# Optimization experiments

Measured on AMD Instinct MI355X. Metric: run time of the kernel, lower is better.

## Reference

```python
import jax, jax.numpy as jnp
import numpy as np

N_NODES = 50000
N_EDGES = 500000
N_GRAPHS = 256
D_IN, D_H1, D_H2, D_H3, D_OUT = 768, 256, 128, 64, 2


def _glorot(key, shape):
    fan_in, fan_out = shape[1], shape[0]
    lim = float(np.sqrt(6.0 / (fan_in + fan_out)))
    return jax.random.uniform(key, shape, jnp.float32, -lim, lim)


def setup_inputs() -> dict:
    key = jax.random.key(0)
    ks = jax.random.split(key, 12)
    x = jax.random.normal(ks[0], (N_NODES, D_IN), jnp.float32)
    edge_index = jax.random.randint(ks[1], (2, N_EDGES), 0, N_NODES, jnp.int64)
    batch = jnp.sort(jax.random.randint(ks[2], (N_NODES,), 0, N_GRAPHS, jnp.int64))
    return {
        "x": x,
        "edge_index": edge_index,
        "batch": batch,
        # SAGEConv1: out = lin_l(mean_aggr) + lin_r(x); bias only on lin_l (PyG default)
        "W1_l": _glorot(ks[3], (D_H1, D_IN)),
        "b1_l": jnp.zeros((D_H1,), jnp.float32),
        "W1_r": _glorot(ks[4], (D_H1, D_IN)),
        # SAGEConv2
        "W2_l": _glorot(ks[5], (D_H2, D_H1)),
        "b2_l": jnp.zeros((D_H2,), jnp.float32),
        "W2_r": _glorot(ks[6], (D_H2, D_H1)),
        # MLP head
        "W3": _glorot(ks[7], (D_H3, D_H2)),
        "b3": jnp.zeros((D_H3,), jnp.float32),
        "W4": _glorot(ks[8], (D_OUT, D_H3)),
        "b4": jnp.zeros((D_OUT,), jnp.float32),
    }


def _sage_conv(x, src, dst, deg_inv, W_l, b_l, W_r):
    # mean aggregation of neighbor features: scatter-add then divide by in-degree
    aggr = jax.ops.segment_sum(x[src], dst, num_segments=N_NODES)  # [N, d]
    aggr = aggr * deg_inv[:, None]
    return aggr @ W_l.T + b_l + x @ W_r.T


def reference(x, edge_index, batch, W1_l, b1_l, W1_r, W2_l, b2_l, W2_r, W3, b3, W4, b4):
    src, dst = edge_index[0], edge_index[1]
    deg = jax.ops.segment_sum(jnp.ones((N_EDGES,), x.dtype), dst, num_segments=N_NODES)
    deg_inv = jnp.where(deg > 0, 1.0 / jnp.maximum(deg, 1.0), 0.0)

    h = jax.nn.relu(_sage_conv(x, src, dst, deg_inv, W1_l, b1_l, W1_r))
    h = jax.nn.relu(_sage_conv(h, src, dst, deg_inv, W2_l, b2_l, W2_r))

    # global_mean_pool over graph ids
    pooled = jax.ops.segment_sum(h, batch, num_segments=N_GRAPHS)  # [G, 128]
    cnt = jax.ops.segment_sum(jnp.ones((N_NODES,), h.dtype), batch, num_segments=N_GRAPHS)
    pooled = pooled / jnp.maximum(cnt, 1.0)[:, None]

    # dropout is identity in eval mode
    h = pooled @ W3.T + b3
    h = h @ W4.T + b4
    return jax.nn.softmax(h, axis=-1)
```

## Files before the change

kernel.cpp:

```cpp
#include <hip/hip_runtime.h>
#include <cstdint>
#include <cstddef>

#define N_NODES 50000
#define N_EDGES 500000
#define N_GRAPHS 256
#define D_IN 768
#define D_H1 256
#define D_H2 128

typedef __attribute__((ext_vector_type(8))) __bf16 bf16x8;
typedef __attribute__((ext_vector_type(4))) float f32x4;

__device__ __forceinline__ float bf2f(uint32_t u) {
    union { uint32_t i; float f; } v; v.i = u << 16; return v.f;
}
__device__ __forceinline__ uint32_t f2bf(float f) {
    union { float f; uint32_t i; } v; v.f = f;
    uint32_t u = v.i;
    return (u + 0x7FFFu + ((u >> 16) & 1u)) >> 16;
}

__global__ void k_packA(const float* __restrict__ in, uint16_t* __restrict__ out,
                        int nchunks, int KT, int K) {
    int c = blockIdx.x * 256 + threadIdx.x;
    if (c >= nchunks) return;
    int l = c & 63, t = c >> 6;
    int kt = t % KT, mt = t / KT;
    int fr = l & 15, fq = l >> 4;
    const float* p = in + (size_t)(mt * 16 + fr) * K + kt * 32 + fq * 8;
    float4 u = *(const float4*)p, v = *(const float4*)(p + 4);
    uint4 o;
    o.x = f2bf(u.x) | (f2bf(u.y) << 16);
    o.y = f2bf(u.z) | (f2bf(u.w) << 16);
    o.z = f2bf(v.x) | (f2bf(v.y) << 16);
    o.w = f2bf(v.z) | (f2bf(v.w) << 16);
    *(uint4*)(out + (size_t)c * 8) = o;
}

__global__ void k_packW(const float* __restrict__ inL, const float* __restrict__ inR,
                        uint16_t* __restrict__ out, int rowsL, int nchunks, int KT, int K) {
    int c = blockIdx.x * 256 + threadIdx.x;
    if (c >= nchunks) return;
    int l = c & 63, t = c >> 6;
    int kt = t % KT, mt = t / KT;
    int fr = l & 15, fq = l >> 4;
    int row = mt * 16 + fr;
    const float* src = (row < rowsL) ? (inL + (size_t)row * K) : (inR + (size_t)(row - rowsL) * K);
    const float* p = src + kt * 32 + fq * 8;
    float4 u = *(const float4*)p, v = *(const float4*)(p + 4);
    uint4 o;
    o.x = f2bf(u.x) | (f2bf(u.y) << 16);
    o.y = f2bf(u.z) | (f2bf(u.w) << 16);
    o.z = f2bf(v.x) | (f2bf(v.y) << 16);
    o.w = f2bf(v.z) | (f2bf(v.w) << 16);
    *(uint4*)(out + (size_t)c * 8) = o;
}

__global__ void k_hist(const int* __restrict__ dst, int* __restrict__ deg, int n) {
    int e = blockIdx.x * blockDim.x + threadIdx.x;
    if (e < n) atomicAdd(&deg[dst[e]], 1);
}

__global__ void k_scan1(const int* __restrict__ deg, int* __restrict__ row_ex,
                        int* __restrict__ bsum, int n) {
    __shared__ int buf[256];
    int t = threadIdx.x, i = blockIdx.x * 256 + t;
    int v = (i < n) ? deg[i] : 0;
    buf[t] = v; __syncthreads();
    for (int off = 1; off < 256; off <<= 1) {
        int u = (t >= off) ? buf[t - off] : 0;
        __syncthreads(); buf[t] += u; __syncthreads();
    }
    if (i < n) row_ex[i] = buf[t] - v;
    if (t == 255) bsum[blockIdx.x] = buf[255];
}
__global__ void k_scan2(const int* __restrict__ bsum, int* __restrict__ boff, int nb) {
    __shared__ int buf[256];
    int t = threadIdx.x;
    int v = (t < nb) ? bsum[t] : 0;
    buf[t] = v; __syncthreads();
    for (int off = 1; off < 256; off <<= 1) {
        int u = (t >= off) ? buf[t - off] : 0;
        __syncthreads(); buf[t] += u; __syncthreads();
    }
    if (t < nb) boff[t] = buf[t] - v;
}
__global__ void k_scan3(const int* __restrict__ deg, const int* __restrict__ boff,
                        int* __restrict__ row_start, float* __restrict__ deg_inv, int n) {
    int i = blockIdx.x * 256 + threadIdx.x;
    if (i < n) {
        row_start[i] += boff[blockIdx.x];
        int d = deg[i];
        deg_inv[i] = (d > 0) ? (1.0f / (float)d) : 0.0f;
    }
    if (blockIdx.x == 0 && threadIdx.x == 0) row_start[n] = N_EDGES;
}

__global__ void k_fill(const int* __restrict__ src, const int* __restrict__ dst,
                       const int* __restrict__ row_start, int* __restrict__ cursor,
                       int* __restrict__ csr_src, int n) {
    int e = blockIdx.x * blockDim.x + threadIdx.x;
    if (e < n) {
        int d = dst[e];
        int pos = row_start[d] + atomicAdd(&cursor[d], 1);
        csr_src[pos] = src[e];
    }
}

__global__ __launch_bounds__(256, 2) void k_mgemm(
    const uint16_t* __restrict__ Ap, const uint16_t* __restrict__ Bp,
    uint16_t* __restrict__ C, int M, int N, int KT)
{
    const int tid = threadIdx.x;
    const int wave = tid >> 6, lane = tid & 63;
    const int fr = lane & 15, fq = lane >> 4;
    const int bn = blockIdx.x * 256, bm = blockIdx.y * 128;
    const int wm = (wave >> 1) * 64, wn = (wave & 1) * 128;
    const int mtiles = (M + 15) >> 4;

    const bf16x8* ap[4];
    const bf16x8* bp[8];
    #pragma unroll
    for (int mi = 0; mi < 4; ++mi) {
        int mt = ((bm + wm) >> 4) + mi;
        if (mt > mtiles - 1) mt = mtiles - 1;
        ap[mi] = (const bf16x8*)Ap + (size_t)mt * KT * 64 + lane;
    }
    #pragma unroll
    for (int ni = 0; ni < 8; ++ni) {
        int nt = ((bn + wn) >> 4) + ni;
        bp[ni] = (const bf16x8*)Bp + (size_t)nt * KT * 64 + lane;
    }

    f32x4 acc[4][8] = {};
    bf16x8 a0[4], b0[8], a1[4], b1[8];

    auto lA = [&](int kt, bf16x8* d) {
        #pragma unroll
        for (int mi = 0; mi < 4; ++mi) d[mi] = ap[mi][kt * 64];
    };
    auto lB = [&](int kt, bf16x8* d) {
        #pragma unroll
        for (int ni = 0; ni < 8; ++ni) d[ni] = bp[ni][kt * 64];
    };
    auto step = [&](bf16x8* a, bf16x8* b) {
        #pragma unroll
        for (int mi = 0; mi < 4; ++mi)
            #pragma unroll
            for (int ni = 0; ni < 8; ++ni)
                acc[mi][ni] = __builtin_amdgcn_mfma_f32_16x16x32_bf16(
                    a[mi], b[ni], acc[mi][ni], 0, 0, 0);
    };

    lA(0, a0); lB(0, b0);
    for (int ks = 0; ks < KT; ks += 2) {
        lA(ks + 1, a1); lB(ks + 1, b1);
        step(a0, b0);
        if (ks + 2 < KT) { lA(ks + 2, a0); lB(ks + 2, b0); }
        step(a1, b1);
    }

    #pragma unroll
    for (int mi = 0; mi < 4; ++mi) {
        #pragma unroll
        for (int r = 0; r < 4; ++r) {
            int row = bm + wm + mi * 16 + fq * 4 + r;
            if (row >= M) continue;
            #pragma unroll
            for (int ni = 0; ni < 8; ++ni) {
                int col = bn + wn + ni * 16 + fr;
                C[(size_t)row * N + col] = (uint16_t)f2bf(acc[mi][ni][r]);
            }
        }
    }
}

__global__ __launch_bounds__(256) void k_agg1(
    const uint16_t* __restrict__ y, const int* __restrict__ row_start,
    const int* __restrict__ csr, const float* __restrict__ deg_inv,
    const float* __restrict__ bias, uint16_t* __restrict__ h1p)
{
    int node = blockIdx.x * 8 + (threadIdx.x >> 5);
    if (node >= N_NODES) return;
    int c = threadIdx.x & 31;
    int s = row_start[node], e = row_start[node + 1];
    float a[8] = {};
    int p = s;
    for (; p + 1 < e; p += 2) {
        uint4 t0 = *(const uint4*)(y + (size_t)csr[p] * 512 + c * 8);
        uint4 t1 = *(const uint4*)(y + (size_t)csr[p + 1] * 512 + c * 8);
        a[0] += bf2f(t0.x & 0xFFFF) + bf2f(t1.x & 0xFFFF);
        a[1] += bf2f(t0.x >> 16)    + bf2f(t1.x >> 16);
        a[2] += bf2f(t0.y & 0xFFFF) + bf2f(t1.y & 0xFFFF);
        a[3] += bf2f(t0.y >> 16)    + bf2f(t1.y >> 16);
        a[4] += bf2f(t0.z & 0xFFFF) + bf2f(t1.z & 0xFFFF);
        a[5] += bf2f(t0.z >> 16)    + bf2f(t1.z >> 16);
        a[6] += bf2f(t0.w & 0xFFFF) + bf2f(t1.w & 0xFFFF);
        a[7] += bf2f(t0.w >> 16)    + bf2f(t1.w >> 16);
    }
    if (p < e) {
        uint4 t0 = *(const uint4*)(y + (size_t)csr[p] * 512 + c * 8);
        a[0] += bf2f(t0.x & 0xFFFF); a[1] += bf2f(t0.x >> 16);
        a[2] += bf2f(t0.y & 0xFFFF); a[3] += bf2f(t0.y >> 16);
        a[4] += bf2f(t0.z & 0xFFFF); a[5] += bf2f(t0.z >> 16);
        a[6] += bf2f(t0.w & 0xFFFF); a[7] += bf2f(t0.w >> 16);
    }
    float w = deg_inv[node];
    uint4 tx = *(const uint4*)(y + (size_t)node * 512 + 256 + c * 8);
    float4 b0 = *(const float4*)(bias + c * 8);
    float4 b1 = *(const float4*)(bias + c * 8 + 4);
    float v0 = fmaxf(a[0] * w + bf2f(tx.x & 0xFFFF) + b0.x, 0.f);
    float v1 = fmaxf(a[1] * w + bf2f(tx.x >> 16)    + b0.y, 0.f);
    float v2 = fmaxf(a[2] * w + bf2f(tx.y & 0xFFFF) + b0.z, 0.f);
    float v3 = fmaxf(a[3] * w + bf2f(tx.y >> 16)    + b0.w, 0.f);
    float v4 = fmaxf(a[4] * w + bf2f(tx.z & 0xFFFF) + b1.x, 0.f);
    float v5 = fmaxf(a[5] * w + bf2f(tx.z >> 16)    + b1.y, 0.f);
    float v6 = fmaxf(a[6] * w + bf2f(tx.w & 0xFFFF) + b1.z, 0.f);
    float v7 = fmaxf(a[7] * w + bf2f(tx.w >> 16)    + b1.w, 0.f);
    uint4 o;
    o.x = f2bf(v0) | (f2bf(v1) << 16);
    o.y = f2bf(v2) | (f2bf(v3) << 16);
    o.z = f2bf(v4) | (f2bf(v5) << 16);
    o.w = f2bf(v6) | (f2bf(v7) << 16);
    uint32_t addr = (((node >> 4) * 8 + (c >> 2)) * 64 + (c & 3) * 16 + (node & 15));
    *(uint4*)(h1p + (size_t)addr * 8) = o;
}

__global__ __launch_bounds__(256) void k_agg2(
    const uint16_t* __restrict__ y, const int* __restrict__ row_start,
    const int* __restrict__ csr, const float* __restrict__ deg_inv,
    const float* __restrict__ bias, float* __restrict__ out)
{
    int node = blockIdx.x * 4 + (threadIdx.x >> 6);
    if (node >= N_NODES) return;
    int lane = threadIdx.x & 63;
    int s = row_start[node], e = row_start[node + 1];
    float a0 = 0.f, a1 = 0.f;
    int p = s;
    for (; p + 1 < e; p += 2) {
        uint32_t t0 = *(const uint32_t*)(y + (size_t)csr[p] * 256 + lane * 2);
        uint32_t t1 = *(const uint32_t*)(y + (size_t)csr[p + 1] * 256 + lane * 2);
        a0 += bf2f(t0 & 0xFFFF) + bf2f(t1 & 0xFFFF);
        a1 += bf2f(t0 >> 16)    + bf2f(t1 >> 16);
    }
    if (p < e) {
        uint32_t t0 = *(const uint32_t*)(y + (size_t)csr[p] * 256 + lane * 2);
        a0 += bf2f(t0 & 0xFFFF);
        a1 += bf2f(t0 >> 16);
    }
    float w = deg_inv[node];
    uint32_t tx = *(const uint32_t*)(y + (size_t)node * 256 + 128 + lane * 2);
    float2 b = *(const float2*)(bias + lane * 2);
    float2 o;
    o.x = fmaxf(a0 * w + bf2f(tx & 0xFFFF) + b.x, 0.f);
    o.y = fmaxf(a1 * w + bf2f(tx >> 16)    + b.y, 0.f);
    *(float2*)(out + (size_t)node * 128 + lane * 2) = o;
}

__global__ void k_pool(const float* __restrict__ h2, const int* __restrict__ batch,
                       float* __restrict__ pooled)
{
    int g = blockIdx.x;
    __shared__ int s_lo, s_hi;
    if (threadIdx.x == 0) {
        int lo = 0, hi = N_NODES;
        while (lo < hi) { int m = (lo + hi) >> 1; if (batch[m] < g) lo = m + 1; else hi = m; }
        s_lo = lo;
        int lo2 = lo, hi2 = N_NODES;
        while (lo2 < hi2) { int m = (lo2 + hi2) >> 1; if (batch[m] < g + 1) lo2 = m + 1; else hi2 = m; }
        s_hi = lo2;
    }
    __syncthreads();
    int dim = threadIdx.x;
    float sum = 0.f;
    for (int i = s_lo; i < s_hi; ++i) sum += h2[(size_t)i * D_H2 + dim];
    int cnt = s_hi - s_lo;
    pooled[g * D_H2 + dim] = sum / (float)(cnt > 0 ? cnt : 1);
}

__global__ void k_head(const float* __restrict__ pooled, const float* __restrict__ W3,
                       const float* __restrict__ b3, const float* __restrict__ W4,
                       const float* __restrict__ b4, float* __restrict__ out)
{
    int g = blockIdx.x;
    int j = threadIdx.x;
    __shared__ float p[128];
    __shared__ float hid[64];
    __shared__ float logit[2];
    p[j] = pooled[g * 128 + j];
    p[j + 64] = pooled[g * 128 + 64 + j];
    __syncthreads();
    float s = b3[j];
    #pragma unroll 4
    for (int k = 0; k < 128; ++k) s = fmaf(p[k], W3[j * 128 + k], s);
    hid[j] = s;
    __syncthreads();
    if (j < 2) {
        float l = b4[j];
        for (int k = 0; k < 64; ++k) l = fmaf(hid[k], W4[j * 64 + k], l);
        logit[j] = l;
    }
    __syncthreads();
    if (j == 0) {
        float m = fmaxf(logit[0], logit[1]);
        float e0 = expf(logit[0] - m), e1 = expf(logit[1] - m);
        float inv = 1.0f / (e0 + e1);
        out[g * 2 + 0] = e0 * inv;
        out[g * 2 + 1] = e1 * inv;
    }
}

extern "C" void kernel_launch(void* const* d_in, const int* in_sizes, int n_in,
                              void* d_out, int out_size, void* d_ws, size_t ws_size,
                              hipStream_t stream)
{
    const float* x     = (const float*)d_in[0];
    const int*   ei    = (const int*)d_in[1];
    const int*   batch = (const int*)d_in[2];
    const float* W1l   = (const float*)d_in[3];
    const float* b1l   = (const float*)d_in[4];
    const float* W1r   = (const float*)d_in[5];
    const float* W2l   = (const float*)d_in[6];
    const float* b2l   = (const float*)d_in[7];
    const float* W2r   = (const float*)d_in[8];
    const float* W3    = (const float*)d_in[9];
    const float* b3    = (const float*)d_in[10];
    const float* W4    = (const float*)d_in[11];
    const float* b4    = (const float*)d_in[12];
    float* out = (float*)d_out;

    const int* e_src = ei;
    const int* e_dst = ei + N_EDGES;

    char* ws = (char*)d_ws;
    size_t off = 0;
    auto alloc = [&](size_t bytes) -> void* {
        void* p = ws + off;
        off = (off + bytes + 255) & ~(size_t)255;
        return p;
    };
    int*      deg       = (int*)alloc((size_t)N_NODES * 4);
    int*      row_start = (int*)alloc((size_t)(N_NODES + 1) * 4);
    int*      cursor    = (int*)alloc((size_t)N_NODES * 4);
    int*      csr_src   = (int*)alloc((size_t)N_EDGES * 4);
    float*    deg_inv   = (float*)alloc((size_t)N_NODES * 4);
    int*      bsum      = (int*)alloc(256 * 4);
    int*      boff      = (int*)alloc(256 * 4);
    float*    pooled    = (float*)alloc((size_t)N_GRAPHS * D_H2 * 4);
    uint16_t* W1p       = (uint16_t*)alloc((size_t)512 * 768 * 2);
    uint16_t* W2p       = (uint16_t*)alloc((size_t)256 * 256 * 2);
    uint16_t* xp        = (uint16_t*)alloc((size_t)N_NODES * D_IN * 2);
    uint16_t* y1        = (uint16_t*)alloc((size_t)N_NODES * 512 * 2);
    uint16_t* h1p       = (uint16_t*)alloc((size_t)N_NODES * 256 * 2);

    uint16_t* y2 = xp;
    float*    h2 = (float*)(xp + (size_t)N_NODES * 256);

    hipMemsetAsync(deg, 0, (size_t)N_NODES * 4, stream);
    hipMemsetAsync(cursor, 0, (size_t)N_NODES * 4, stream);

    k_hist<<<(N_EDGES + 255) / 256, 256, 0, stream>>>(e_dst, deg, N_EDGES);
    int nscan = (N_NODES + 255) / 256;
    k_scan1<<<nscan, 256, 0, stream>>>(deg, row_start, bsum, N_NODES);
    k_scan2<<<1, 256, 0, stream>>>(bsum, boff, nscan);
    k_scan3<<<nscan, 256, 0, stream>>>(deg, boff, row_start, deg_inv, N_NODES);
    k_fill<<<(N_EDGES + 255) / 256, 256, 0, stream>>>(e_src, e_dst, row_start, cursor, csr_src, N_EDGES);

    int ncA = 3125 * 24 * 64;
    k_packA<<<(ncA + 255) / 256, 256, 0, stream>>>(x, xp, ncA, 24, 768);
    int ncW1 = 32 * 24 * 64;
    k_packW<<<(ncW1 + 255) / 256, 256, 0, stream>>>(W1l, W1r, W1p, 256, ncW1, 24, 768);
    int ncW2 = 16 * 8 * 64;
    k_packW<<<(ncW2 + 255) / 256, 256, 0, stream>>>(W2l, W2r, W2p, 128, ncW2, 8, 256);

    dim3 g1(2, (N_NODES + 127) / 128);
    k_mgemm<<<g1, 256, 0, stream>>>(xp, W1p, y1, N_NODES, 512, 24);
    k_agg1<<<(N_NODES + 7) / 8, 256, 0, stream>>>(y1, row_start, csr_src, deg_inv, b1l, h1p);

    dim3 g2(1, (N_NODES + 127) / 128);
    k_mgemm<<<g2, 256, 0, stream>>>(h1p, W2p, y2, N_NODES, 256, 8);
    k_agg2<<<(N_NODES + 3) / 4, 256, 0, stream>>>(y2, row_start, csr_src, deg_inv, b2l, h2);

    k_pool<<<N_GRAPHS, 128, 0, stream>>>(h2, batch, pooled);
    k_head<<<N_GRAPHS, 64, 0, stream>>>(pooled, W3, b3, W4, b4, out);
}
```

Before: 529.1 us.

## Fuse preprocessing kernels and overlap CSR fill with first GEMM

Several small kernels are merged into fewer launches. The pack kernels and the degree histogram share one grid, scan2 and scan3 become one kernel, and pool and head become one kernel. The CSR fill now runs as extra blocks inside the first GEMM launch so the two overlap, and the GEMM output is split into separate left and right halves with a grouped block order for reuse. The goal is to cut launch overhead and idle tails between small kernels; the cost is added branch complexity and heterogeneous blocks sharing one launch.

New measurement: 486.8 us. -8.0%, faster.

```diff
diff --git a/kernel.cpp b/kernel.cpp
--- a/kernel.cpp
+++ b/kernel.cpp
@@ -21,14 +21,8 @@
     return (u + 0x7FFFu + ((u >> 16) & 1u)) >> 16;
 }
 
-__global__ void k_packA(const float* __restrict__ in, uint16_t* __restrict__ out,
-                        int nchunks, int KT, int K) {
-    int c = blockIdx.x * 256 + threadIdx.x;
-    if (c >= nchunks) return;
-    int l = c & 63, t = c >> 6;
-    int kt = t % KT, mt = t / KT;
-    int fr = l & 15, fq = l >> 4;
-    const float* p = in + (size_t)(mt * 16 + fr) * K + kt * 32 + fq * 8;
+__device__ __forceinline__ void pack_chunk(const float* __restrict__ p,
+                                           uint16_t* __restrict__ out, int c) {
     float4 u = *(const float4*)p, v = *(const float4*)(p + 4);
     uint4 o;
     o.x = f2bf(u.x) | (f2bf(u.y) << 16);
@@ -38,28 +32,45 @@
     *(uint4*)(out + (size_t)c * 8) = o;
 }
 
-__global__ void k_packW(const float* __restrict__ inL, const float* __restrict__ inR,
-                        uint16_t* __restrict__ out, int rowsL, int nchunks, int KT, int K) {
-    int c = blockIdx.x * 256 + threadIdx.x;
-    if (c >= nchunks) return;
-    int l = c & 63, t = c >> 6;
-    int kt = t % KT, mt = t / KT;
-    int fr = l & 15, fq = l >> 4;
-    int row = mt * 16 + fr;
-    const float* src = (row < rowsL) ? (inL + (size_t)row * K) : (inR + (size_t)(row - rowsL) * K);
-    const float* p = src + kt * 32 + fq * 8;
-    float4 u = *(const float4*)p, v = *(const float4*)(p + 4);
-    uint4 o;
-    o.x = f2bf(u.x) | (f2bf(u.y) << 16);
-    o.y = f2bf(u.z) | (f2bf(u.w) << 16);
-    o.z = f2bf(v.x) | (f2bf(v.y) << 16);
-    o.w = f2bf(v.z) | (f2bf(v.w) << 16);
-    *(uint4*)(out + (size_t)c * 8) = o;
-}
-
-__global__ void k_hist(const int* __restrict__ dst, int* __restrict__ deg, int n) {
-    int e = blockIdx.x * blockDim.x + threadIdx.x;
-    if (e < n) atomicAdd(&deg[dst[e]], 1);
+#define PACKA_BLKS 18750
+#define PACKW1_BLKS 192
+#define PACKW2_BLKS 32
+#define HIST_BLKS 1954
+__global__ __launch_bounds__(256) void k_pack_hist(
+    const float* __restrict__ x, uint16_t* __restrict__ xp,
+    const float* __restrict__ W1l, const float* __restrict__ W1r, uint16_t* __restrict__ W1p,
+    const float* __restrict__ W2l, const float* __restrict__ W2r, uint16_t* __restrict__ W2p,
+    const int* __restrict__ e_dst, int* __restrict__ deg)
+{
+    int b = blockIdx.x;
+    if (b < PACKA_BLKS) {
+        int c = b * 256 + threadIdx.x;
+        int l = c & 63, t = c >> 6;
+        int kt = t % 24, mt = t / 24;
+        int fr = l & 15, fq = l >> 4;
+        pack_chunk(x + (size_t)(mt * 16 + fr) * 768 + kt * 32 + fq * 8, xp, c);
+    } else if (b < PACKA_BLKS + PACKW1_BLKS) {
+        int c = (b - PACKA_BLKS) * 256 + threadIdx.x;
+        int l = c & 63, t = c >> 6;
+        int kt = t % 24, mt = t / 24;
+        int fr = l & 15, fq = l >> 4;
+        int row = mt * 16 + fr;
+        const float* src = (row < 256) ? (W1l + (size_t)row * 768)
+                                       : (W1r + (size_t)(row - 256) * 768);
+        pack_chunk(src + kt * 32 + fq * 8, W1p, c);
+    } else if (b < PACKA_BLKS + PACKW1_BLKS + PACKW2_BLKS) {
+        int c = (b - PACKA_BLKS - PACKW1_BLKS) * 256 + threadIdx.x;
+        int l = c & 63, t = c >> 6;
+        int kt = t % 8, mt = t / 8;
+        int fr = l & 15, fq = l >> 4;
+        int row = mt * 16 + fr;
+        const float* src = (row < 128) ? (W2l + (size_t)row * 256)
+                                       : (W2r + (size_t)(row - 128) * 256);
+        pack_chunk(src + kt * 32 + fq * 8, W2p, c);
+    } else {
+        int e = (b - PACKA_BLKS - PACKW1_BLKS - PACKW2_BLKS) * 256 + threadIdx.x;
+        if (e < N_EDGES) atomicAdd(&deg[e_dst[e]], 1);
+    }
 }
 
 __global__ void k_scan1(const int* __restrict__ deg, int* __restrict__ row_ex,
@@ -75,7 +86,9 @@
     if (i < n) row_ex[i] = buf[t] - v;
     if (t == 255) bsum[blockIdx.x] = buf[255];
 }
-__global__ void k_scan2(const int* __restrict__ bsum, int* __restrict__ boff, int nb) {
+__global__ void k_scan23(const int* __restrict__ deg, const int* __restrict__ bsum,
+                         int* __restrict__ row_start, float* __restrict__ deg_inv,
+                         int n, int nb) {
     __shared__ int buf[256];
     int t = threadIdx.x;
     int v = (t < nb) ? bsum[t] : 0;
@@ -84,27 +97,101 @@
         int u = (t >= off) ? buf[t - off] : 0;
         __syncthreads(); buf[t] += u; __syncthreads();
     }
-    if (t < nb) boff[t] = buf[t] - v;
-}
-__global__ void k_scan3(const int* __restrict__ deg, const int* __restrict__ boff,
-                        int* __restrict__ row_start, float* __restrict__ deg_inv, int n) {
-    int i = blockIdx.x * 256 + threadIdx.x;
+    int b = blockIdx.x;
+    int boff = buf[b] - ((b < nb) ? bsum[b] : 0);
+    int i = b * 256 + t;
     if (i < n) {
-        row_start[i] += boff[blockIdx.x];
+        row_start[i] += boff;
         int d = deg[i];
         deg_inv[i] = (d > 0) ? (1.0f / (float)d) : 0.0f;
     }
-    if (blockIdx.x == 0 && threadIdx.x == 0) row_start[n] = N_EDGES;
-}
-
-__global__ void k_fill(const int* __restrict__ src, const int* __restrict__ dst,
-                       const int* __restrict__ row_start, int* __restrict__ cursor,
-                       int* __restrict__ csr_src, int n) {
-    int e = blockIdx.x * blockDim.x + threadIdx.x;
-    if (e < n) {
-        int d = dst[e];
-        int pos = row_start[d] + atomicAdd(&cursor[d], 1);
-        csr_src[pos] = src[e];
+    if (b == 0 && t == 0) row_start[n] = N_EDGES;
+}
+
+#define G1_BLKS 784
+__global__ __launch_bounds__(256, 2) void k_gemm1_fill(
+    const uint16_t* __restrict__ Ap, const uint16_t* __restrict__ Bp,
+    uint16_t* __restrict__ Cl, uint16_t* __restrict__ Cr,
+    const int* __restrict__ e_src, const int* __restrict__ e_dst,
+    const int* __restrict__ row_start, int* __restrict__ cursor,
+    int* __restrict__ csr_src)
+{
+    if (blockIdx.x >= G1_BLKS) {
+        int e = (blockIdx.x - G1_BLKS) * 256 + threadIdx.x;
+        if (e < N_EDGES) {
+            int d = e_dst[e];
+            int pos = row_start[d] + atomicAdd(&cursor[d], 1);
+            csr_src[pos] = e_src[e];
+        }
+        return;
+    }
+    const int i = blockIdx.x;
+    const int pr = (i >> 4) * 8 + (i & 7);
+    const int half = (i >> 3) & 1;
+    if (pr >= 391) return;
+    const int KT = 24, M = N_NODES;
+    const int tid = threadIdx.x;
+    const int wave = tid >> 6, lane = tid & 63;
+    const int fr = lane & 15, fq = lane >> 4;
+    const int bm = pr * 128;
+    const int wm = (wave >> 1) * 64, wn = (wave & 1) * 128;
+    const int mtiles = (M + 15) >> 4;
+
+    const bf16x8* ap[4];
+    const bf16x8* bp[8];
+    #pragma unroll
+    for (int mi = 0; mi < 4; ++mi) {
+        int mt = ((bm + wm) >> 4) + mi;
+        if (mt > mtiles - 1) mt = mtiles - 1;
+        ap[mi] = (const bf16x8*)Ap + (size_t)mt * KT * 64 + lane;
+    }
+    #pragma unroll
+    for (int ni = 0; ni < 8; ++ni) {
+        int nt = ((half * 256 + wn) >> 4) + ni;
+        bp[ni] = (const bf16x8*)Bp + (size_t)nt * KT * 64 + lane;
+    }
+
+    f32x4 acc[4][8] = {};
+    bf16x8 a0[4], b0[8], a1[4], b1[8];
+
+    auto lA = [&](int kt, bf16x8* d) {
+        #pragma unroll
+        for (int mi = 0; mi < 4; ++mi) d[mi] = ap[mi][kt * 64];
+    };
+    auto lB = [&](int kt, bf16x8* d) {
+        #pragma unroll
+        for (int ni = 0; ni < 8; ++ni) d[ni] = bp[ni][kt * 64];
+    };
+    auto step = [&](bf16x8* a, bf16x8* b) {
+        #pragma unroll
+        for (int mi = 0; mi < 4; ++mi)
+            #pragma unroll
+            for (int ni = 0; ni < 8; ++ni)
+                acc[mi][ni] = __builtin_amdgcn_mfma_f32_16x16x32_bf16(
+                    a[mi], b[ni], acc[mi][ni], 0, 0, 0);
+    };
+
+    lA(0, a0); lB(0, b0);
+    for (int ks = 0; ks < KT; ks += 2) {
+        lA(ks + 1, a1); lB(ks + 1, b1);
+        step(a0, b0);
+        if (ks + 2 < KT) { lA(ks + 2, a0); lB(ks + 2, b0); }
+        step(a1, b1);
+    }
+
+    uint16_t* __restrict__ C = half ? Cr : Cl;
+    #pragma unroll
+    for (int mi = 0; mi < 4; ++mi) {
+        #pragma unroll
+        for (int r = 0; r < 4; ++r) {
+            int row = bm + wm + mi * 16 + fq * 4 + r;
+            if (row >= M) continue;
+            #pragma unroll
+            for (int ni = 0; ni < 8; ++ni) {
+                int col = wn + ni * 16 + fr;
+                C[(size_t)row * 256 + col] = (uint16_t)f2bf(acc[mi][ni][r]);
+            }
+        }
     }
 }
 
@@ -177,9 +264,10 @@
 }
 
 __global__ __launch_bounds__(256) void k_agg1(
-    const uint16_t* __restrict__ y, const int* __restrict__ row_start,
-    const int* __restrict__ csr, const float* __restrict__ deg_inv,
-    const float* __restrict__ bias, uint16_t* __restrict__ h1p)
+    const uint16_t* __restrict__ yl, const uint16_t* __restrict__ yr,
+    const int* __restrict__ row_start, const int* __restrict__ csr,
+    const float* __restrict__ deg_inv, const float* __restrict__ bias,
+    uint16_t* __restrict__ h1p)
 {
     int node = blockIdx.x * 8 + (threadIdx.x >> 5);
     if (node >= N_NODES) return;
@@ -188,8 +276,8 @@
     float a[8] = {};
     int p = s;
     for (; p + 1 < e; p += 2) {
-        uint4 t0 = *(const uint4*)(y + (size_t)csr[p] * 512 + c * 8);
-        uint4 t1 = *(const uint4*)(y + (size_t)csr[p + 1] * 512 + c * 8);
+        uint4 t0 = *(const uint4*)(yl + (size_t)csr[p] * 256 + c * 8);
+        uint4 t1 = *(const uint4*)(yl + (size_t)csr[p + 1] * 256 + c * 8);
         a[0] += bf2f(t0.x & 0xFFFF) + bf2f(t1.x & 0xFFFF);
         a[1] += bf2f(t0.x >> 16)    + bf2f(t1.x >> 16);
         a[2] += bf2f(t0.y & 0xFFFF) + bf2f(t1.y & 0xFFFF);
@@ -200,14 +288,14 @@
         a[7] += bf2f(t0.w >> 16)    + bf2f(t1.w >> 16);
     }
     if (p < e) {
-        uint4 t0 = *(const uint4*)(y + (size_t)csr[p] * 512 + c * 8);
+        uint4 t0 = *(const uint4*)(yl + (size_t)csr[p] * 256 + c * 8);
         a[0] += bf2f(t0.x & 0xFFFF); a[1] += bf2f(t0.x >> 16);
         a[2] += bf2f(t0.y & 0xFFFF); a[3] += bf2f(t0.y >> 16);
         a[4] += bf2f(t0.z & 0xFFFF); a[5] += bf2f(t0.z >> 16);
         a[6] += bf2f(t0.w & 0xFFFF); a[7] += bf2f(t0.w >> 16);
     }
     float w = deg_inv[node];
-    uint4 tx = *(const uint4*)(y + (size_t)node * 512 + 256 + c * 8);
+    uint4 tx = *(const uint4*)(yr + (size_t)node * 256 + c * 8);
     float4 b0 = *(const float4*)(bias + c * 8);
     float4 b1 = *(const float4*)(bias + c * 8 + 4);
     float v0 = fmaxf(a[0] * w + bf2f(tx.x & 0xFFFF) + b0.x, 0.f);
@@ -258,12 +346,18 @@
     *(float2*)(out + (size_t)node * 128 + lane * 2) = o;
 }
 
-__global__ void k_pool(const float* __restrict__ h2, const int* __restrict__ batch,
-                       float* __restrict__ pooled)
+__global__ void k_poolhead(const float* __restrict__ h2, const int* __restrict__ batch,
+                           const float* __restrict__ W3, const float* __restrict__ b3,
+                           const float* __restrict__ W4, const float* __restrict__ b4,
+                           float* __restrict__ out)
 {
     int g = blockIdx.x;
     __shared__ int s_lo, s_hi;
-    if (threadIdx.x == 0) {
+    __shared__ float p[128];
+    __shared__ float hid[64];
+    __shared__ float logit[2];
+    int t = threadIdx.x;
+    if (t == 0) {
         int lo = 0, hi = N_NODES;
         while (lo < hi) { int m = (lo + hi) >> 1; if (batch[m] < g) lo = m + 1; else hi = m; }
         s_lo = lo;
@@ -272,37 +366,25 @@
         s_hi = lo2;
     }
     __syncthreads();
-    int dim = threadIdx.x;
     float sum = 0.f;
-    for (int i = s_lo; i < s_hi; ++i) sum += h2[(size_t)i * D_H2 + dim];
+    for (int i = s_lo; i < s_hi; ++i) sum += h2[(size_t)i * D_H2 + t];
     int cnt = s_hi - s_lo;
-    pooled[g * D_H2 + dim] = sum / (float)(cnt > 0 ? cnt : 1);
-}
-
-__global__ void k_head(const float* __restrict__ pooled, const float* __restrict__ W3,
-                       const float* __restrict__ b3, const float* __restrict__ W4,
-                       const float* __restrict__ b4, float* __restrict__ out)
-{
-    int g = blockIdx.x;
-    int j = threadIdx.x;
-    __shared__ float p[128];
-    __shared__ float hid[64];
-    __shared__ float logit[2];
-    p[j] = pooled[g * 128 + j];
-    p[j + 64] = pooled[g * 128 + 64 + j];
+    p[t] = sum / (float)(cnt > 0 ? cnt : 1);
     __syncthreads();
-    float s = b3[j];
-    #pragma unroll 4
-    for (int k = 0; k < 128; ++k) s = fmaf(p[k], W3[j * 128 + k], s);
-    hid[j] = s;
+    if (t < 64) {
+        float s = b3[t];
+        #pragma unroll 4
+        for (int k = 0; k < 128; ++k) s = fmaf(p[k], W3[t * 128 + k], s);
+        hid[t] = s;
+    }
     __syncthreads();
-    if (j < 2) {
-        float l = b4[j];
-        for (int k = 0; k < 64; ++k) l = fmaf(hid[k], W4[j * 64 + k], l);
-        logit[j] = l;
+    if (t < 2) {
+        float l = b4[t];
+        for (int k = 0; k < 64; ++k) l = fmaf(hid[k], W4[t * 64 + k], l);
+        logit[t] = l;
     }
     __syncthreads();
-    if (j == 0) {
+    if (t == 0) {
         float m = fmaxf(logit[0], logit[1]);
         float e0 = expf(logit[0] - m), e1 = expf(logit[1] - m);
         float inv = 1.0f / (e0 + e1);
@@ -340,48 +422,39 @@
         off = (off + bytes + 255) & ~(size_t)255;
         return p;
     };
-    int*      deg       = (int*)alloc((size_t)N_NODES * 4);
+    int*      deg       = (int*)alloc((size_t)2 * N_NODES * 4);
+    int*      cursor    = deg + N_NODES;
     int*      row_start = (int*)alloc((size_t)(N_NODES + 1) * 4);
-    int*      cursor    = (int*)alloc((size_t)N_NODES * 4);
     int*      csr_src   = (int*)alloc((size_t)N_EDGES * 4);
     float*    deg_inv   = (float*)alloc((size_t)N_NODES * 4);
     int*      bsum      = (int*)alloc(256 * 4);
-    int*      boff      = (int*)alloc(256 * 4);
-    float*    pooled    = (float*)alloc((size_t)N_GRAPHS * D_H2 * 4);
     uint16_t* W1p       = (uint16_t*)alloc((size_t)512 * 768 * 2);
     uint16_t* W2p       = (uint16_t*)alloc((size_t)256 * 256 * 2);
     uint16_t* xp        = (uint16_t*)alloc((size_t)N_NODES * D_IN * 2);
     uint16_t* y1        = (uint16_t*)alloc((size_t)N_NODES * 512 * 2);
     uint16_t* h1p       = (uint16_t*)alloc((size_t)N_NODES * 256 * 2);
 
+    uint16_t* y1l = y1;
+    uint16_t* y1r = y1 + (size_t)N_NODES * 256;
     uint16_t* y2 = xp;
     float*    h2 = (float*)(xp + (size_t)N_NODES * 256);
 
-    hipMemsetAsync(deg, 0, (size_t)N_NODES * 4, stream);
-    hipMemsetAsync(cursor, 0, (size_t)N_NODES * 4, stream);
-
-    k_hist<<<(N_EDGES + 255) / 256, 256, 0, stream>>>(e_dst, deg, N_EDGES);
+    hipMemsetAsync(deg, 0, (size_t)2 * N_NODES * 4, stream);
+
+    k_pack_hist<<<PACKA_BLKS + PACKW1_BLKS + PACKW2_BLKS + HIST_BLKS, 256, 0, stream>>>(
+        x, xp, W1l, W1r, W1p, W2l, W2r, W2p, e_dst, deg);
+
     int nscan = (N_NODES + 255) / 256;
     k_scan1<<<nscan, 256, 0, stream>>>(deg, row_start, bsum, N_NODES);
-    k_scan2<<<1, 256, 0, stream>>>(bsum, boff, nscan);
-    k_scan3<<<nscan, 256, 0, stream>>>(deg, boff, row_start, deg_inv, N_NODES);
-    k_fill<<<(N_EDGES + 255) / 256, 256, 0, stream>>>(e_src, e_dst, row_start, cursor, csr_src, N_EDGES);
-
-    int ncA = 3125 * 24 * 64;
-    k_packA<<<(ncA + 255) / 256, 256, 0, stream>>>(x, xp, ncA, 24, 768);
-    int ncW1 = 32 * 24 * 64;
-    k_packW<<<(ncW1 + 255) / 256, 256, 0, stream>>>(W1l, W1r, W1p, 256, ncW1, 24, 768);
-    int ncW2 = 16 * 8 * 64;
-    k_packW<<<(ncW2 + 255) / 256, 256, 0, stream>>>(W2l, W2r, W2p, 128, ncW2, 8, 256);
-
-    dim3 g1(2, (N_NODES + 127) / 128);
-    k_mgemm<<<g1, 256, 0, stream>>>(xp, W1p, y1, N_NODES, 512, 24);
-    k_agg1<<<(N_NODES + 7) / 8, 256, 0, stream>>>(y1, row_start, csr_src, deg_inv, b1l, h1p);
+    k_scan23<<<nscan, 256, 0, stream>>>(deg, bsum, row_start, deg_inv, N_NODES, nscan);
+
+    k_gemm1_fill<<<G1_BLKS + HIST_BLKS, 256, 0, stream>>>(
+        xp, W1p, y1l, y1r, e_src, e_dst, row_start, cursor, csr_src);
+    k_agg1<<<(N_NODES + 7) / 8, 256, 0, stream>>>(y1l, y1r, row_start, csr_src, deg_inv, b1l, h1p);
 
     dim3 g2(1, (N_NODES + 127) / 128);
     k_mgemm<<<g2, 256, 0, stream>>>(h1p, W2p, y2, N_NODES, 256, 8);
     k_agg2<<<(N_NODES + 3) / 4, 256, 0, stream>>>(y2, row_start, csr_src, deg_inv, b2l, h2);
 
-    k_pool<<<N_GRAPHS, 128, 0, stream>>>(h2, batch, pooled);
-    k_head<<<N_GRAPHS, 64, 0, stream>>>(pooled, W3, b3, W4, b4, out);
-}
+    k_poolhead<<<N_GRAPHS, 128, 0, stream>>>(h2, batch, W3, b3, W4, b4, out);
+}
```
